# Kernel tuning notes

Hardware: AMD Instinct MI355X
Metric: run time of the kernel (lower is better)

## Reference

```python
import jax, jax.numpy as jnp
import numpy as np

B, P, E, H, U = 64, 256, 256, 8, 6
HD = E // H            # head_dim = 32
TOPK = 32
DFF = 4 * E
EPS_LN = 1e-5
EPS_RMS = 1.1920929e-07  # torch.finfo(float32).eps (RMSNorm default eps)
NEG = -1e9


def setup_inputs() -> dict:
    key = jax.random.key(0)
    ks = jax.random.split(key, 10)
    s = 0.02
    f32 = jnp.float32
    return {
        "x": jax.random.normal(ks[0], (B, P, E), f32),
        "u": jax.random.normal(ks[1], (B, U, P, P), f32),
        "norm1_w": jnp.ones((E,), f32),
        "norm1_b": jnp.zeros((E,), f32),
        "wq": jax.random.normal(ks[2], (E, E), f32) * s,
        "wk": jax.random.normal(ks[3], (E, E), f32) * s,
        "wv": jax.random.normal(ks[4], (E, E), f32) * s,
        "wo": jax.random.normal(ks[5], (E, E), f32) * s,
        "bo": jnp.zeros((E,), f32),
        "uw": jax.random.normal(ks[6], (H, U), f32) * s,  # 1x1 Conv2d(u_embed->H)
        "ub": jnp.zeros((H,), f32),
        "norm2_w": jnp.ones((E,), f32),
        "norm2_b": jnp.zeros((E,), f32),
        "rms_w": jnp.ones((E,), f32),
        "w1": jax.random.normal(ks[7], (E, DFF), f32) * s,
        "b1": jnp.zeros((DFF,), f32),
        "w2": jax.random.normal(ks[8], (DFF, E), f32) * s,
        "b2": jnp.zeros((E,), f32),
    }


def _layernorm(x, w, b):
    m = jnp.mean(x, axis=-1, keepdims=True)
    v = jnp.mean(jnp.square(x - m), axis=-1, keepdims=True)
    return (x - m) * jax.lax.rsqrt(v + EPS_LN) * w + b


def reference(x, u, norm1_w, norm1_b, wq, wk, wv, wo, bo, uw, ub,
              norm2_w, norm2_b, rms_w, w1, b1, w2, b2):
    xn = _layernorm(x, norm1_w, norm1_b)
    # projections -> [B, H, P, HD]
    q = (xn @ wq).reshape(B, P, H, HD).transpose(0, 2, 1, 3)
    k = (xn @ wk).reshape(B, P, H, HD).transpose(0, 2, 1, 3)
    v = (xn @ wv).reshape(B, P, H, HD).transpose(0, 2, 1, 3)
    scores = jnp.einsum('bhqd,bhkd->bhqk', q, k) * (HD ** -0.5)

    # 1x1 conv bias over pairwise features: [B, U, P, P] -> [B, H, P, P]
    uh = jnp.einsum('bupq,hu->bhpq', u, uw) + ub[None, :, None, None]

    # top-k sparse mask from edge importance (sum of |bias| over heads)
    imp = jnp.abs(uh).sum(axis=1)                    # [B, P, P]
    kk = min(TOPK, P - 1)
    _, idx = jax.lax.top_k(imp, kk)                  # [B, P, kk]
    mask = jnp.zeros((B, P, P), dtype=bool).at[
        jnp.arange(B)[:, None, None],
        jnp.arange(P)[None, :, None],
        idx,
    ].set(True)
    uh = jnp.where(mask[:, None, :, :], uh, NEG)

    attn = jax.nn.softmax(scores + uh, axis=-1)
    attn = jnp.nan_to_num(attn, nan=0.0)

    ctx = jnp.einsum('bhqk,bhkd->bhqd', attn, v)
    ctx = ctx.transpose(0, 2, 1, 3).reshape(B, P, E)
    attn_out = ctx @ wo + bo

    h = _layernorm(attn_out, norm2_w, norm2_b) + x
    hn = h * jax.lax.rsqrt(jnp.mean(h * h, axis=-1, keepdims=True) + EPS_RMS) * rms_w
    z = jax.nn.silu(hn @ w1 + b1) @ w2 + b2
    return z + h, attn
```

## Files before the change

kernel.cpp:

```cpp
#include <hip/hip_runtime.h>
#include <hip/hip_bf16.h>

typedef unsigned short u16;
typedef unsigned long long u64;
typedef __attribute__((ext_vector_type(8))) short short8;
typedef __attribute__((ext_vector_type(4))) short s16x4;
typedef __attribute__((ext_vector_type(4))) float f32x4;

#define NB 64
#define NP 256
#define NE 256
#define NH 8
#define NHD 32
#define NU 6
#define NDFF 1024
#define NM (NB*NP)

__device__ __forceinline__ u16 f2bf(float f) {
  unsigned u = __float_as_uint(f);
  unsigned r = 0x7fffu + ((u >> 16) & 1u);
  return (u16)((u + r) >> 16);
}
__device__ __forceinline__ float bf2f(u16 v) {
  return __uint_as_float(((unsigned)v) << 16);
}

__device__ __forceinline__ void gl_lds16(const u16* g, u16* l) {
  __builtin_amdgcn_global_load_lds(
      (const __attribute__((address_space(1))) unsigned int*)g,
      (__attribute__((address_space(3))) unsigned int*)l, 16, 0, 0);
}

__global__ __launch_bounds__(256) void k_prep(
    const float* __restrict__ wq, const float* __restrict__ wk, const float* __restrict__ wv,
    const float* __restrict__ wo, const float* __restrict__ w1, const float* __restrict__ w2,
    u16* __restrict__ wqkvT, u16* __restrict__ woT, u16* __restrict__ w1T, u16* __restrict__ w2T) {
  __shared__ float tile[32][33];
  int bid = blockIdx.x;
  const float* src; u16* dst; int R, C, tr, tc;
  if (bid < 192)      { int m = bid >> 6, t = bid & 63; src = m==0?wq:(m==1?wk:wv); dst = wqkvT + m*256*256; R=256; C=256;  tr=t>>3; tc=t&7;  }
  else if (bid < 256) { int t = bid-192; src=wo; dst=woT; R=256;  C=256;  tr=t>>3; tc=t&7;  }
  else if (bid < 512) { int t = bid-256; src=w1; dst=w1T; R=256;  C=1024; tr=t>>5; tc=t&31; }
  else                { int t = bid-512; src=w2; dst=w2T; R=1024; C=256;  tr=t>>3; tc=t&7;  }
  int r0 = tr*32, c0 = tc*32;
  int rr = threadIdx.x >> 5, cc = threadIdx.x & 31;
  #pragma unroll
  for (int p = 0; p < 4; p++)
    tile[rr + p*8][cc] = src[(size_t)(r0 + rr + p*8) * C + c0 + cc];
  __syncthreads();
  #pragma unroll
  for (int p = 0; p < 4; p++)
    dst[(size_t)(c0 + rr + p*8) * R + r0 + cc] = f2bf(tile[cc][rr + p*8]);
}

__global__ __launch_bounds__(256) void k_ln1(
    const float* __restrict__ x, const float* __restrict__ w, const float* __restrict__ b,
    u16* __restrict__ xn) {
  int row = blockIdx.x * 4 + (threadIdx.x >> 6);
  int lane = threadIdx.x & 63;
  float4 v = *(const float4*)(x + (size_t)row * NE + lane * 4);
  float s = v.x + v.y + v.z + v.w;
  #pragma unroll
  for (int o = 32; o; o >>= 1) s += __shfl_xor(s, o);
  float mean = s * (1.f / 256.f);
  float d0 = v.x - mean, d1 = v.y - mean, d2 = v.z - mean, d3 = v.w - mean;
  float q = d0*d0 + d1*d1 + d2*d2 + d3*d3;
  #pragma unroll
  for (int o = 32; o; o >>= 1) q += __shfl_xor(q, o);
  float r = rsqrtf(q * (1.f / 256.f) + 1e-5f);
  int c = lane * 4;
  ushort4 o4;
  o4.x = f2bf(d0 * r * w[c+0] + b[c+0]);
  o4.y = f2bf(d1 * r * w[c+1] + b[c+1]);
  o4.z = f2bf(d2 * r * w[c+2] + b[c+2]);
  o4.w = f2bf(d3 * r * w[c+3] + b[c+3]);
  *(ushort4*)(xn + (size_t)row * NE + c) = o4;
}

template<class Epi>
__global__ __launch_bounds__(256, 4) void k_gemm128(
    const u16* __restrict__ A, const u16* __restrict__ BT, int K, Epi epi) {
  __shared__ __align__(16) u16 As[128 * 32];
  __shared__ __align__(16) u16 Bs[128 * 32];
  const int t = threadIdx.x;
  const int m0 = blockIdx.x * 128, n0 = blockIdx.y * 128;
  const int lane = t & 63, wv = t >> 6;
  const int fr = lane & 15, fg = lane >> 4;
  const int wm = (wv >> 1) * 64, wn = (wv & 1) * 64;
  const int row = t >> 2;
  const int gs = (t & 3) ^ ((row >> 1) & 3);
  const u16* Ap = A + (size_t)(m0 + row) * K + gs * 8;
  const u16* Bp = BT + (size_t)(n0 + row) * K + gs * 8;
  u16* lA = As + wv * 512;
  u16* lB = Bs + wv * 512;
  f32x4 acc[4][4] = {};
  for (int k0 = 0; k0 < K; k0 += 32) {
    __syncthreads();
    gl_lds16(Ap + k0, lA);
    gl_lds16(Ap + k0 + (size_t)64 * K, lA + 2048);
    gl_lds16(Bp + k0, lB);
    gl_lds16(Bp + k0 + (size_t)64 * K, lB + 2048);
    __syncthreads();
    short8 a[4], b[4];
    #pragma unroll
    for (int i = 0; i < 4; i++) {
      int ra = wm + i * 16 + fr;
      a[i] = *(const short8*)(As + ra * 32 + ((fg ^ ((ra >> 1) & 3)) << 3));
    }
    #pragma unroll
    for (int j = 0; j < 4; j++) {
      int rb = wn + j * 16 + fr;
      b[j] = *(const short8*)(Bs + rb * 32 + ((fg ^ ((rb >> 1) & 3)) << 3));
    }
    #pragma unroll
    for (int i = 0; i < 4; i++)
      #pragma unroll
      for (int j = 0; j < 4; j++)
        acc[i][j] = __builtin_amdgcn_mfma_f32_16x16x32_bf16(a[i], b[j], acc[i][j], 0, 0, 0);
  }
  #pragma unroll
  for (int i = 0; i < 4; i++)
    #pragma unroll
    for (int j = 0; j < 4; j++)
      #pragma unroll
      for (int jj = 0; jj < 4; jj++)
        epi(m0 + wm + i * 16 + fg * 4 + jj, n0 + wn + j * 16 + fr, acc[i][j][jj]);
}

struct EpiQKV {
  u16 *q, *k, *vT;
  __device__ __forceinline__ void operator()(int m, int n, float v) const {
    int b = m >> 8, p = m & 255;
    int h = (n >> 5) & 7, d = n & 31;
    u16 bv = f2bf(v);
    if (n < 256)       q [(((size_t)(b*NH + h)) * NP + p) * NHD + d] = bv;
    else if (n < 512)  k [(((size_t)(b*NH + h)) * NP + p) * NHD + d] = bv;
    else               vT[(((size_t)(b*NH + h)) * NHD + d) * NP + p] = bv;
  }
};
struct EpiWo {
  const float* bo; float* ao;
  __device__ __forceinline__ void operator()(int m, int n, float v) const {
    ao[(size_t)m * NE + n] = v + bo[n];
  }
};
struct EpiFFN1 {
  const float* b1; u16* tb;
  __device__ __forceinline__ void operator()(int m, int n, float v) const {
    float s = v + b1[n];
    tb[(size_t)m * NDFF + n] = f2bf(s / (1.f + __expf(-s)));
  }
};
struct EpiFFN2 {
  const float* b2; const float* hb; float* out0;
  __device__ __forceinline__ void operator()(int m, int n, float v) const {
    out0[(size_t)m * NE + n] = v + b2[n] + hb[(size_t)m * NE + n];
  }
};

__global__ __launch_bounds__(512, 2) void k_fattn(
    const float* __restrict__ u, const float* __restrict__ uw, const float* __restrict__ ub,
    const u16* __restrict__ qb, const u16* __restrict__ kb, const u16* __restrict__ vTb,
    float* __restrict__ attn, u16* __restrict__ ctx) {
  __shared__ __align__(16) u16 bias[NH * 16 * 256];
  const int i0 = blockIdx.x;
  const int b = (i0 & 7) * 8 + ((i0 >> 3) & 7);
  const int r0 = (i0 >> 6) << 4;
  const int w = threadIdx.x >> 6;
  const int lane = threadIdx.x & 63;
  const int fr = lane & 15, fg = lane >> 4;
  const u16 NEGBF = f2bf(-1e9f);

  for (int rr = 0; rr < 2; rr++) {
    const int p = r0 + 2 * w + rr;
    const int rl = 2 * w + rr;
    const float* up = u + ((size_t)b * NU * NP + p) * NP + lane * 4;
    float4 uv[NU];
    #pragma unroll
    for (int uu = 0; uu < NU; uu++) uv[uu] = *(const float4*)(up + (size_t)uu * NP * NP);
    double imp[4] = {0.0, 0.0, 0.0, 0.0};
    #pragma unroll
    for (int h = 0; h < NH; h++) {
      double s0 = (double)ub[h], s1 = s0, s2 = s0, s3 = s0;
      #pragma unroll
      for (int uu = 0; uu < NU; uu++) {
        double ww = (double)uw[h * NU + uu];
        s0 += ww * (double)uv[uu].x;
        s1 += ww * (double)uv[uu].y;
        s2 += ww * (double)uv[uu].z;
        s3 += ww * (double)uv[uu].w;
      }
      imp[0] += fabs(s0); imp[1] += fabs(s1); imp[2] += fabs(s2); imp[3] += fabs(s3);
      ushort4 o;
      o.x = f2bf((float)s0); o.y = f2bf((float)s1);
      o.z = f2bf((float)s2); o.w = f2bf((float)s3);
      *(ushort4*)(bias + (h * 16 + rl) * 256 + lane * 4) = o;
    }
    u64 ib0 = (u64)__double_as_longlong(imp[0]);
    u64 ib1 = (u64)__double_as_longlong(imp[1]);
    u64 ib2 = (u64)__double_as_longlong(imp[2]);
    u64 ib3 = (u64)__double_as_longlong(imp[3]);
    u64 res = 0;
    for (int bit = 62; bit >= 0; --bit) {
      u64 cand = res | (1ull << bit);
      int cnt = __popcll(__ballot(ib0 >= cand)) + __popcll(__ballot(ib1 >= cand))
              + __popcll(__ballot(ib2 >= cand)) + __popcll(__ballot(ib3 >= cand));
      if (cnt >= 32) res = cand;
    }
    bool k0 = ib0 >= res, k1 = ib1 >= res, k2 = ib2 >= res, k3 = ib3 >= res;
    #pragma unroll
    for (int h = 0; h < NH; h++) {
      ushort4* pp = (ushort4*)(bias + (h * 16 + rl) * 256 + lane * 4);
      ushort4 v = *pp;
      if (!k0) v.x = NEGBF;
      if (!k1) v.y = NEGBF;
      if (!k2) v.z = NEGBF;
      if (!k3) v.w = NEGBF;
      *pp = v;
    }
  }
  __syncthreads();

  const size_t bh = (size_t)b * NH + w;
  const u16* qp = qb + (bh * NP + r0) * NHD;
  short8 af = *(const short8*)(qp + fr * NHD + fg * 8);
  const u16* kp = kb + bh * NP * NHD;
  u16* ps = bias + w * 4096;
  const float scale = 0.17677669529663687f;

  float mx[4] = {-3e38f, -3e38f, -3e38f, -3e38f};
  #pragma unroll
  for (int nb = 0; nb < 16; nb++) {
    short8 bfr = *(const short8*)(kp + (nb * 16 + fr) * NHD + fg * 8);
    f32x4 z = {0.f, 0.f, 0.f, 0.f};
    z = __builtin_amdgcn_mfma_f32_16x16x32_bf16(af, bfr, z, 0, 0, 0);
    #pragma unroll
    for (int jj = 0; jj < 4; jj++)
      mx[jj] = fmaxf(mx[jj], z[jj] * scale + bf2f(ps[(fg * 4 + jj) * 256 + nb * 16 + fr]));
  }
  #pragma unroll
  for (int o = 1; o < 16; o <<= 1)
    #pragma unroll
    for (int jj = 0; jj < 4; jj++) mx[jj] = fmaxf(mx[jj], __shfl_xor(mx[jj], o));

  float sum[4] = {0.f, 0.f, 0.f, 0.f};
  #pragma unroll
  for (int nb = 0; nb < 16; nb++) {
    short8 bfr = *(const short8*)(kp + (nb * 16 + fr) * NHD + fg * 8);
    f32x4 z = {0.f, 0.f, 0.f, 0.f};
    z = __builtin_amdgcn_mfma_f32_16x16x32_bf16(af, bfr, z, 0, 0, 0);
    #pragma unroll
    for (int jj = 0; jj < 4; jj++) {
      int idx = (fg * 4 + jj) * 256 + nb * 16 + fr;
      float e = __expf(z[jj] * scale + bf2f(ps[idx]) - mx[jj]);
      sum[jj] += e;
      ps[idx] = f2bf(e);
    }
  }
  #pragma unroll
  for (int o = 1; o < 16; o <<= 1)
    #pragma unroll
    for (int jj = 0; jj < 4; jj++) sum[jj] += __shfl_xor(sum[jj], o);
  float inv[4];
  #pragma unroll
  for (int jj = 0; jj < 4; jj++) inv[jj] = 1.f / sum[jj];

  s16x4 rowv[16];
  #pragma unroll
  for (int i = 0; i < 16; i++) rowv[i] = *(const s16x4*)(ps + i * 256 + lane * 4);
  float* ab = attn + (bh * NP + r0) * NP;
  #pragma unroll
  for (int i = 0; i < 16; i++) {
    float iv = __shfl(inv[i & 3], (i >> 2) << 4);
    float4 o;
    o.x = bf2f((u16)rowv[i][0]) * iv;
    o.y = bf2f((u16)rowv[i][1]) * iv;
    o.z = bf2f((u16)rowv[i][2]) * iv;
    o.w = bf2f((u16)rowv[i][3]) * iv;
    *(float4*)(ab + i * NP + lane * 4) = o;
  }
  const int g = lane >> 1, sub = lane & 1;
  #pragma unroll
  for (int i = 0; i < 16; i++)
    *(s16x4*)(ps + i * 256 + ((g ^ (i & 7)) << 3) + sub * 4) = rowv[i];

  const u16* vp = vTb + bh * NHD * NP;
  f32x4 c0 = {0.f, 0.f, 0.f, 0.f}, c1 = {0.f, 0.f, 0.f, 0.f};
  #pragma unroll
  for (int kk = 0; kk < 8; kk++) {
    short8 pa = *(const short8*)(ps + fr * 256 + (((kk * 4 + fg) ^ (fr & 7)) << 3));
    short8 v0 = *(const short8*)(vp + fr * NP + kk * 32 + fg * 8);
    short8 v1 = *(const short8*)(vp + (16 + fr) * NP + kk * 32 + fg * 8);
    c0 = __builtin_amdgcn_mfma_f32_16x16x32_bf16(pa, v0, c0, 0, 0, 0);
    c1 = __builtin_amdgcn_mfma_f32_16x16x32_bf16(pa, v1, c1, 0, 0, 0);
  }
  #pragma unroll
  for (int jj = 0; jj < 4; jj++) {
    int prow = r0 + fg * 4 + jj;
    u16* crow = ctx + ((size_t)(b * NP + prow)) * NE + w * NHD;
    crow[fr]      = f2bf(c0[jj] * inv[jj]);
    crow[16 + fr] = f2bf(c1[jj] * inv[jj]);
  }
}

__global__ __launch_bounds__(256) void k_ln2rms(
    const float* __restrict__ ao, const float* __restrict__ x,
    const float* __restrict__ w, const float* __restrict__ b, const float* __restrict__ rw,
    float* __restrict__ hbuf, u16* __restrict__ hn) {
  int row = blockIdx.x * 4 + (threadIdx.x >> 6);
  int lane = threadIdx.x & 63;
  float4 v = *(const float4*)(ao + (size_t)row * NE + lane * 4);
  float s = v.x + v.y + v.z + v.w;
  #pragma unroll
  for (int o = 32; o; o >>= 1) s += __shfl_xor(s, o);
  float mean = s * (1.f / 256.f);
  float d0 = v.x - mean, d1 = v.y - mean, d2 = v.z - mean, d3 = v.w - mean;
  float q = d0*d0 + d1*d1 + d2*d2 + d3*d3;
  #pragma unroll
  for (int o = 32; o; o >>= 1) q += __shfl_xor(q, o);
  float r = rsqrtf(q * (1.f / 256.f) + 1e-5f);
  float4 xv = *(const float4*)(x + (size_t)row * NE + lane * 4);
  int c = lane * 4;
  float h0 = d0 * r * w[c+0] + b[c+0] + xv.x;
  float h1 = d1 * r * w[c+1] + b[c+1] + xv.y;
  float h2 = d2 * r * w[c+2] + b[c+2] + xv.z;
  float h3 = d3 * r * w[c+3] + b[c+3] + xv.w;
  *(float4*)(hbuf + (size_t)row * NE + c) = make_float4(h0, h1, h2, h3);
  float ss = h0*h0 + h1*h1 + h2*h2 + h3*h3;
  #pragma unroll
  for (int o = 32; o; o >>= 1) ss += __shfl_xor(ss, o);
  float rm = rsqrtf(ss * (1.f / 256.f) + 1.1920929e-07f);
  ushort4 o4;
  o4.x = f2bf(h0 * rm * rw[c+0]);
  o4.y = f2bf(h1 * rm * rw[c+1]);
  o4.z = f2bf(h2 * rm * rw[c+2]);
  o4.w = f2bf(h3 * rm * rw[c+3]);
  *(ushort4*)(hn + (size_t)row * NE + c) = o4;
}

extern "C" void kernel_launch(void* const* d_in, const int* in_sizes, int n_in,
                              void* d_out, int out_size, void* d_ws, size_t ws_size,
                              hipStream_t stream) {
  (void)in_sizes; (void)n_in; (void)out_size; (void)ws_size;
  const float* x    = (const float*)d_in[0];
  const float* u    = (const float*)d_in[1];
  const float* n1w  = (const float*)d_in[2];
  const float* n1b  = (const float*)d_in[3];
  const float* wq   = (const float*)d_in[4];
  const float* wk   = (const float*)d_in[5];
  const float* wv   = (const float*)d_in[6];
  const float* wo   = (const float*)d_in[7];
  const float* bo   = (const float*)d_in[8];
  const float* uw   = (const float*)d_in[9];
  const float* ub   = (const float*)d_in[10];
  const float* n2w  = (const float*)d_in[11];
  const float* n2b  = (const float*)d_in[12];
  const float* rmsw = (const float*)d_in[13];
  const float* w1   = (const float*)d_in[14];
  const float* b1   = (const float*)d_in[15];
  const float* w2   = (const float*)d_in[16];
  const float* b2   = (const float*)d_in[17];
  float* out0 = (float*)d_out;
  float* attn = out0 + (size_t)NM * NE;
  char* ws = (char*)d_ws;
  u16* wqkvT = (u16*)(ws + 0x000000);
  u16* woT   = (u16*)(ws + 0x060000);
  u16* w1T   = (u16*)(ws + 0x080000);
  u16* w2T   = (u16*)(ws + 0x100000);
  u16* qb    = (u16*)(ws + 0x200000);
  u16* kb    = (u16*)(ws + 0xA00000);
  u16* vTb   = (u16*)(ws + 0x1200000);
  u16* xn    = (u16*)(ws + 0x1A00000);
  u16* ctx   = (u16*)(ws + 0x2200000);
  float* ao  = (float*)(ws + 0x2A00000);
  float* hb  = (float*)(ws + 0x3A00000);
  u16* hn    = (u16*)(ws + 0x4A00000);
  u16* tb    = (u16*)(ws + 0x200000);

  k_prep<<<dim3(768), dim3(256), 0, stream>>>(wq, wk, wv, wo, w1, w2, wqkvT, woT, w1T, w2T);
  k_ln1<<<dim3(NM/4), dim3(256), 0, stream>>>(x, n1w, n1b, xn);
  k_gemm128<<<dim3(NM/128, 768/128), dim3(256), 0, stream>>>(xn, wqkvT, NE, EpiQKV{qb, kb, vTb});
  k_fattn<<<dim3(NB*16), dim3(512), 0, stream>>>(u, uw, ub, qb, kb, vTb, attn, ctx);
  k_gemm128<<<dim3(NM/128, NE/128), dim3(256), 0, stream>>>(ctx, woT, NE, EpiWo{bo, ao});
  k_ln2rms<<<dim3(NM/4), dim3(256), 0, stream>>>(ao, x, n2w, n2b, rmsw, hb, hn);
  k_gemm128<<<dim3(NM/128, NDFF/128), dim3(256), 0, stream>>>(hn, w1T, NE, EpiFFN1{b1, tb});
  k_gemm128<<<dim3(NM/128, NE/128), dim3(256), 0, stream>>>(tb, w2T, NDFF, EpiFFN2{b2, hb, out0});
}
```

Before: 423.0 us.

## Stage GEMM epilogue through LDS for vectorized stores; split V projection transposed

The GEMM epilogue now writes the accumulators to a padded shared-memory tile as bf16, then each thread reads 8 contiguous values and stores them with 128-bit vector writes. Before, each element was a scalar store. The V projection becomes a separate GEMM with the operands swapped, so its transposed layout comes out directly and can use contiguous vector stores instead of scattered stride-256 writes. As a trade-off, fp32 outputs (attention projection, FFN2) are rounded to bf16 before the bias/residual add, which loses precision. The larger LDS footprint also lowers the launch-bounds occupancy hint from 4 to 3.

```diff
diff --git a/kernel.cpp b/kernel.cpp
--- a/kernel.cpp
+++ b/kernel.cpp
@@ -78,10 +78,11 @@
 }
 
 template<class Epi>
-__global__ __launch_bounds__(256, 4) void k_gemm128(
+__global__ __launch_bounds__(256, 3) void k_gemm128(
     const u16* __restrict__ A, const u16* __restrict__ BT, int K, Epi epi) {
-  __shared__ __align__(16) u16 As[128 * 32];
-  __shared__ __align__(16) u16 Bs[128 * 32];
+  __shared__ __align__(16) u16 smem[128 * 132];
+  u16* As = smem;
+  u16* Bs = smem + 4096;
   const int t = threadIdx.x;
   const int m0 = blockIdx.x * 128, n0 = blockIdx.y * 128;
   const int lane = t & 63, wv = t >> 6;
@@ -118,43 +119,77 @@
       for (int j = 0; j < 4; j++)
         acc[i][j] = __builtin_amdgcn_mfma_f32_16x16x32_bf16(a[i], b[j], acc[i][j], 0, 0, 0);
   }
+  __syncthreads();
   #pragma unroll
   for (int i = 0; i < 4; i++)
     #pragma unroll
     for (int j = 0; j < 4; j++)
       #pragma unroll
       for (int jj = 0; jj < 4; jj++)
-        epi(m0 + wm + i * 16 + fg * 4 + jj, n0 + wn + j * 16 + fr, acc[i][j][jj]);
-}
-
-struct EpiQKV {
-  u16 *q, *k, *vT;
-  __device__ __forceinline__ void operator()(int m, int n, float v) const {
+        smem[(wm + i * 16 + fg * 4 + jj) * 132 + wn + j * 16 + fr] = f2bf(acc[i][j][jj]);
+  __syncthreads();
+  #pragma unroll
+  for (int rr = 0; rr < 8; rr++) {
+    int rl = rr * 16 + (t >> 4);
+    int c0 = (t & 15) * 8;
+    short8 v = *(const short8*)(smem + rl * 132 + c0);
+    epi.vec(m0 + rl, n0 + c0, v);
+  }
+}
+
+struct EpiQK {
+  u16 *q, *k;
+  __device__ __forceinline__ void vec(int m, int n, short8 v) const {
     int b = m >> 8, p = m & 255;
-    int h = (n >> 5) & 7, d = n & 31;
-    u16 bv = f2bf(v);
-    if (n < 256)       q [(((size_t)(b*NH + h)) * NP + p) * NHD + d] = bv;
-    else if (n < 512)  k [(((size_t)(b*NH + h)) * NP + p) * NHD + d] = bv;
-    else               vT[(((size_t)(b*NH + h)) * NHD + d) * NP + p] = bv;
+    u16* dst = (n < 256)
+      ? q + ((((size_t)(b*NH + (n >> 5))) * NP + p) * NHD + (n & 31))
+      : k + ((((size_t)(b*NH + ((n - 256) >> 5))) * NP + p) * NHD + (n & 31));
+    *(short8*)dst = v;
+  }
+};
+struct EpiVT {
+  u16* vT;
+  __device__ __forceinline__ void vec(int m, int n, short8 v) const {
+    int h = m >> 5, d = m & 31, b = n >> 8, p0 = n & 255;
+    *(short8*)(vT + (((size_t)(b*NH + h)) * NHD + d) * NP + p0) = v;
   }
 };
 struct EpiWo {
   const float* bo; float* ao;
-  __device__ __forceinline__ void operator()(int m, int n, float v) const {
-    ao[(size_t)m * NE + n] = v + bo[n];
+  __device__ __forceinline__ void vec(int m, int n, short8 v) const {
+    float* dst = ao + (size_t)m * NE + n;
+    float4 o0, o1;
+    o0.x = bf2f((u16)v[0]) + bo[n+0]; o0.y = bf2f((u16)v[1]) + bo[n+1];
+    o0.z = bf2f((u16)v[2]) + bo[n+2]; o0.w = bf2f((u16)v[3]) + bo[n+3];
+    o1.x = bf2f((u16)v[4]) + bo[n+4]; o1.y = bf2f((u16)v[5]) + bo[n+5];
+    o1.z = bf2f((u16)v[6]) + bo[n+6]; o1.w = bf2f((u16)v[7]) + bo[n+7];
+    *(float4*)dst = o0; *(float4*)(dst + 4) = o1;
   }
 };
 struct EpiFFN1 {
   const float* b1; u16* tb;
-  __device__ __forceinline__ void operator()(int m, int n, float v) const {
-    float s = v + b1[n];
-    tb[(size_t)m * NDFF + n] = f2bf(s / (1.f + __expf(-s)));
+  __device__ __forceinline__ void vec(int m, int n, short8 v) const {
+    short8 o;
+    #pragma unroll
+    for (int i = 0; i < 8; i++) {
+      float s = bf2f((u16)v[i]) + b1[n + i];
+      o[i] = (short)f2bf(s / (1.f + __expf(-s)));
+    }
+    *(short8*)(tb + (size_t)m * NDFF + n) = o;
   }
 };
 struct EpiFFN2 {
   const float* b2; const float* hb; float* out0;
-  __device__ __forceinline__ void operator()(int m, int n, float v) const {
-    out0[(size_t)m * NE + n] = v + b2[n] + hb[(size_t)m * NE + n];
+  __device__ __forceinline__ void vec(int m, int n, short8 v) const {
+    const float* hp = hb + (size_t)m * NE + n;
+    float4 h0 = *(const float4*)hp, h1 = *(const float4*)(hp + 4);
+    float4 o0, o1;
+    o0.x = bf2f((u16)v[0]) + b2[n+0] + h0.x; o0.y = bf2f((u16)v[1]) + b2[n+1] + h0.y;
+    o0.z = bf2f((u16)v[2]) + b2[n+2] + h0.z; o0.w = bf2f((u16)v[3]) + b2[n+3] + h0.w;
+    o1.x = bf2f((u16)v[4]) + b2[n+4] + h1.x; o1.y = bf2f((u16)v[5]) + b2[n+5] + h1.y;
+    o1.z = bf2f((u16)v[6]) + b2[n+6] + h1.z; o1.w = bf2f((u16)v[7]) + b2[n+7] + h1.w;
+    float* dst = out0 + (size_t)m * NE + n;
+    *(float4*)dst = o0; *(float4*)(dst + 4) = o1;
   }
 };
 
@@ -379,7 +414,8 @@
 
   k_prep<<<dim3(768), dim3(256), 0, stream>>>(wq, wk, wv, wo, w1, w2, wqkvT, woT, w1T, w2T);
   k_ln1<<<dim3(NM/4), dim3(256), 0, stream>>>(x, n1w, n1b, xn);
-  k_gemm128<<<dim3(NM/128, 768/128), dim3(256), 0, stream>>>(xn, wqkvT, NE, EpiQKV{qb, kb, vTb});
+  k_gemm128<<<dim3(NM/128, 512/128), dim3(256), 0, stream>>>(xn, wqkvT, NE, EpiQK{qb, kb});
+  k_gemm128<<<dim3(256/128, NM/128), dim3(256), 0, stream>>>(wqkvT + 512*256, xn, NE, EpiVT{vTb});
   k_fattn<<<dim3(NB*16), dim3(512), 0, stream>>>(u, uw, ub, qb, kb, vTb, attn, ctx);
   k_gemm128<<<dim3(NM/128, NE/128), dim3(256), 0, stream>>>(ctx, woT, NE, EpiWo{bo, ao});
   k_ln2rms<<<dim3(NM/4), dim3(256), 0, stream>>>(ao, x, n2w, n2b, rmsw, hb, hn);
```

Measured after the change: 403.5 us. 4.6% less time.
